# Optimization experiments

Hardware: AMD Instinct MI355X
Metric: run time of the kernel (lower is better)

Reference implementation:

```python
import jax, jax.numpy as jnp
import numpy as np

N_POS = 8192          # number of positive samples
N_NEG = 4000          # negatives per positive
N_TOT = N_POS + N_POS * N_NEG


def setup_inputs() -> dict:
    key = jax.random.key(0)
    k1, k2 = jax.random.split(key)
    predict_val = jax.random.normal(k1, (N_TOT,), dtype=jnp.float32)
    # 'index' is a permutation; the module reorders predict_val by argsort(index)
    index = jax.random.permutation(k2, jnp.arange(N_TOT, dtype=jnp.int64))
    return {"predict_val": predict_val, "index": index, "num": N_NEG, "num_pos": N_POS}


def reference(predict_val, index, num, num_pos):
    # index_tuple = sorted(enumerate(index)) by value -> reorder by argsort(index)
    pv = predict_val[jnp.argsort(index)]
    pos = pv[:num_pos]                                  # [num_pos]
    neg = pv[num_pos:num_pos + num_pos * num]
    neg = neg.reshape(num_pos, num)                     # [num_pos, num]
    # rank of pos among {neg, pos} sorted descending == 1 + #(neg > pos)
    # (ties are randomly broken in the original; measure-zero for continuous scores)
    rank = 1 + jnp.sum(neg > pos[:, None], axis=-1)     # [num_pos], int
    sample_mrr = 1.0 / rank.astype(pv.dtype)            # [num_pos]
    mrr = jnp.mean(sample_mrr)
    return mrr, sample_mrr
```

## Files before the change

### kernel.cpp

```cpp
#include <hip/hip_runtime.h>


constexpr int N_POS = 8192;
constexpr int N_NEG = 4000;
constexpr int NSLOT = N_POS / 4;
constexpr int GRID  = 256;
constexpr int BLK   = 1024;
constexpr int NTHR  = GRID * BLK;
constexpr int NITER = 32;
constexpr int CNT_BLOCKS = 512;

typedef int   vint4   __attribute__((ext_vector_type(4)));
typedef float vfloat4 __attribute__((ext_vector_type(4)));
typedef unsigned int u32;
typedef unsigned long long u64;

__global__ __launch_bounds__(BLK, 4) void fused_mrr_kernel(
    const vint4* __restrict__ idx4, const float* __restrict__ pvs,
    float* __restrict__ pos, u64* __restrict__ cnt, u32* __restrict__ bar,
    float* __restrict__ out, int nvec) {
  __shared__ float pos_lds[N_POS];
  __shared__ u32   lcnt[N_POS];
  __shared__ float wsum[BLK / 64];
  __shared__ int   is_last;
  const int tid = threadIdx.x;
  const int gid = blockIdx.x * BLK + tid;
  const vfloat4* __restrict__ pv4 = (const vfloat4*)pvs;

#pragma unroll
  for (int i = 0; i < N_POS / BLK; ++i) lcnt[tid + i * BLK] = 0u;
  if (gid <= NSLOT) (void)atomicExch(&cnt[gid], 0ull);

  u32 code[2 * NITER];
#define PA_ELEM(VX, PIDX, CO)                                            \
  {                                                                      \
    u32 c_ = ((VX) >= N_POS) ? ((u32)((VX)-N_POS) / (u32)N_NEG)          \
                             : 0xFFFFu;                                  \
    if ((VX) < N_POS) (void)atomicExch(&pos[VX], pvs[PIDX]);             \
    (CO) = c_;                                                           \
  }
#pragma unroll
  for (int i = 0; i < NITER; ++i) {
    const int j = gid + i * NTHR;
    if (j < nvec) {
      vint4 v = __builtin_nontemporal_load(&idx4[j]);
      u32 c0, c1, c2, c3;
      PA_ELEM(v.x, 4 * j + 0, c0)
      PA_ELEM(v.y, 4 * j + 1, c1)
      PA_ELEM(v.z, 4 * j + 2, c2)
      PA_ELEM(v.w, 4 * j + 3, c3)
      code[2 * i]     = c0 | (c1 << 16);
      code[2 * i + 1] = c2 | (c3 << 16);
    } else {
      code[2 * i]     = 0xFFFFFFFFu;
      code[2 * i + 1] = 0xFFFFFFFFu;
    }
  }
  for (int j = gid + NITER * NTHR; j < nvec; j += NTHR) {
    vint4 v = idx4[j];
    u32 dummy;
    PA_ELEM(v.x, 4 * j + 0, dummy)
    PA_ELEM(v.y, 4 * j + 1, dummy)
    PA_ELEM(v.z, 4 * j + 2, dummy)
    PA_ELEM(v.w, 4 * j + 3, dummy)
    (void)dummy;
  }
#undef PA_ELEM

  __builtin_amdgcn_s_waitcnt(0);
  __syncthreads();
  if (tid == 0) {
    __hip_atomic_fetch_add(bar, 1u, __ATOMIC_RELAXED,
                           __HIP_MEMORY_SCOPE_AGENT);
    while (__hip_atomic_load(bar, __ATOMIC_RELAXED,
                             __HIP_MEMORY_SCOPE_AGENT) < (u32)GRID)
      __builtin_amdgcn_s_sleep(4);
  }
  __syncthreads();

#pragma unroll
  for (int i = 0; i < N_POS / BLK; ++i) {
    const int s = tid + i * BLK;
    pos_lds[s] = __hip_atomic_load(&pos[s], __ATOMIC_RELAXED,
                                   __HIP_MEMORY_SCOPE_AGENT);
  }
  __syncthreads();

#define PB_ELEM(R, XV)                                                   \
  if ((R) < (u32)N_POS && (XV) > pos_lds[R]) atomicAdd(&lcnt[R], 1u);
#pragma unroll
  for (int i = 0; i < NITER; ++i) {
    const int j = gid + i * NTHR;
    if (j < nvec) {
      vfloat4 x = __builtin_nontemporal_load(&pv4[j]);
      u32 w0 = code[2 * i], w1 = code[2 * i + 1];
      u32 r0 = w0 & 0xFFFFu, r1 = w0 >> 16;
      u32 r2 = w1 & 0xFFFFu, r3 = w1 >> 16;
      PB_ELEM(r0, x.x)
      PB_ELEM(r1, x.y)
      PB_ELEM(r2, x.z)
      PB_ELEM(r3, x.w)
    }
  }
  for (int j = gid + NITER * NTHR; j < nvec; j += NTHR) {
    vint4 v = idx4[j];
    vfloat4 x = pv4[j];
    u32 r0 = (v.x >= N_POS) ? ((u32)(v.x - N_POS) / (u32)N_NEG) : 0xFFFFu;
    u32 r1 = (v.y >= N_POS) ? ((u32)(v.y - N_POS) / (u32)N_NEG) : 0xFFFFu;
    u32 r2 = (v.z >= N_POS) ? ((u32)(v.z - N_POS) / (u32)N_NEG) : 0xFFFFu;
    u32 r3 = (v.w >= N_POS) ? ((u32)(v.w - N_POS) / (u32)N_NEG) : 0xFFFFu;
    PB_ELEM(r0, x.x)
    PB_ELEM(r1, x.y)
    PB_ELEM(r2, x.z)
    PB_ELEM(r3, x.w)
  }
#undef PB_ELEM
  __syncthreads();

  for (int s = tid; s < NSLOT; s += BLK) {
    u32 c0 = lcnt[4 * s + 0], c1 = lcnt[4 * s + 1];
    u32 c2 = lcnt[4 * s + 2], c3 = lcnt[4 * s + 3];
    u64 p = (u64)c0 | ((u64)c1 << 16) | ((u64)c2 << 32) | ((u64)c3 << 48);
    if (p) atomicAdd(&cnt[s], p);
  }

  __builtin_amdgcn_s_waitcnt(0);
  __syncthreads();
  if (tid == 0) {
    u64 prev = __hip_atomic_fetch_add(&cnt[NSLOT], 1ull, __ATOMIC_RELAXED,
                                      __HIP_MEMORY_SCOPE_AGENT);
    is_last = (prev == (u64)(GRID - 1));
  }
  __syncthreads();
  if (!is_last) return;

  float lsum = 0.f;
  for (int s = tid; s < NSLOT; s += BLK) {
    u64 p = __hip_atomic_load(&cnt[s], __ATOMIC_RELAXED,
                              __HIP_MEMORY_SCOPE_AGENT);
    float m0 = 1.0f / (float)(1u + (u32)(p & 0xFFFFu));
    float m1 = 1.0f / (float)(1u + (u32)((p >> 16) & 0xFFFFu));
    float m2 = 1.0f / (float)(1u + (u32)((p >> 32) & 0xFFFFu));
    float m3 = 1.0f / (float)(1u + (u32)((p >> 48) & 0xFFFFu));
    vfloat4 m = {m0, m1, m2, m3};
    *(vfloat4*)&out[1 + 4 * s] = m;
    lsum += m0 + m1 + m2 + m3;
  }
#pragma unroll
  for (int off = 32; off > 0; off >>= 1) lsum += __shfl_down(lsum, off, 64);
  if ((tid & 63) == 0) wsum[tid >> 6] = lsum;
  __syncthreads();
  if (tid == 0) {
    float tot = 0.f;
#pragma unroll
    for (int w = 0; w < BLK / 64; ++w) tot += wsum[w];
    out[0] = tot / (float)N_POS;
  }
}

__global__ __launch_bounds__(256) void scatter_pos_kernel(
    const vint4* __restrict__ idx4, const float* __restrict__ pv,
    float* __restrict__ pos, u64* __restrict__ cnt, int nvec) {
  const int gtid = blockIdx.x * 256 + threadIdx.x;
  if (gtid <= NSLOT) cnt[gtid] = 0ull;
  const int stride = gridDim.x * 256;
  int j = gtid;
#define SC_ELEM(V, JJ)                                   \
  if ((V).x < N_POS) pos[(V).x] = pv[4 * (JJ) + 0];      \
  if ((V).y < N_POS) pos[(V).y] = pv[4 * (JJ) + 1];      \
  if ((V).z < N_POS) pos[(V).z] = pv[4 * (JJ) + 2];      \
  if ((V).w < N_POS) pos[(V).w] = pv[4 * (JJ) + 3];
  for (; j + stride < nvec; j += 2 * stride) {
    vint4 a = idx4[j];
    vint4 b = idx4[j + stride];
    SC_ELEM(a, j)
    SC_ELEM(b, j + stride)
  }
  for (; j < nvec; j += stride) {
    vint4 a = idx4[j];
    SC_ELEM(a, j)
  }
#undef SC_ELEM
}

__global__ __launch_bounds__(1024) void count_kernel(
    const vint4* __restrict__ idx4, const vfloat4* __restrict__ pv4,
    const float* __restrict__ pos, u64* __restrict__ cnt,
    float* __restrict__ out, int nvec) {
  __shared__ float pos_lds[N_POS];
  __shared__ u32   lcnt[N_POS];
  __shared__ float wsum[16];
  __shared__ int is_last;
  for (int i = threadIdx.x; i < N_POS; i += 1024) {
    pos_lds[i] = pos[i];
    lcnt[i] = 0u;
  }
  __syncthreads();

  const int stride = gridDim.x * 1024;
  int j = blockIdx.x * 1024 + threadIdx.x;
#define CT_ELEM(IV, XV)                                              \
  if ((IV) >= N_POS) {                                               \
    unsigned r = (unsigned)((IV) - N_POS) / (unsigned)N_NEG;         \
    if ((XV) > pos_lds[r]) atomicAdd(&lcnt[r], 1u);                  \
  }
#define CT_VEC(V, X)                                                 \
  CT_ELEM((V).x, (X).x) CT_ELEM((V).y, (X).y)                        \
  CT_ELEM((V).z, (X).z) CT_ELEM((V).w, (X).w)
  for (; j + stride < nvec; j += 2 * stride) {
    vint4 va = idx4[j];
    vint4 vb = idx4[j + stride];
    vfloat4 xa = __builtin_nontemporal_load(&pv4[j]);
    vfloat4 xb = __builtin_nontemporal_load(&pv4[j + stride]);
    CT_VEC(va, xa)
    CT_VEC(vb, xb)
  }
  for (; j < nvec; j += stride) {
    vint4 va = idx4[j];
    vfloat4 xa = __builtin_nontemporal_load(&pv4[j]);
    CT_VEC(va, xa)
  }
#undef CT_VEC
#undef CT_ELEM
  __syncthreads();

  for (int s = threadIdx.x; s < NSLOT; s += 1024) {
    u32 c0 = lcnt[4 * s + 0], c1 = lcnt[4 * s + 1];
    u32 c2 = lcnt[4 * s + 2], c3 = lcnt[4 * s + 3];
    u64 p = (u64)c0 | ((u64)c1 << 16) | ((u64)c2 << 32) | ((u64)c3 << 48);
    if (p) atomicAdd(&cnt[s], p);
  }

  __builtin_amdgcn_s_waitcnt(0);
  __syncthreads();
  if (threadIdx.x == 0) {
    u64 prev = __hip_atomic_fetch_add(&cnt[NSLOT], 1ull, __ATOMIC_RELAXED,
                                      __HIP_MEMORY_SCOPE_AGENT);
    is_last = (prev == (u64)(gridDim.x - 1));
  }
  __syncthreads();
  if (!is_last) return;

  float lsum = 0.f;
  for (int s = threadIdx.x; s < NSLOT; s += 1024) {
    u64 p = __hip_atomic_load(&cnt[s], __ATOMIC_RELAXED,
                              __HIP_MEMORY_SCOPE_AGENT);
    float m0 = 1.0f / (float)(1u + (u32)(p & 0xFFFFu));
    float m1 = 1.0f / (float)(1u + (u32)((p >> 16) & 0xFFFFu));
    float m2 = 1.0f / (float)(1u + (u32)((p >> 32) & 0xFFFFu));
    float m3 = 1.0f / (float)(1u + (u32)((p >> 48) & 0xFFFFu));
    vfloat4 m = {m0, m1, m2, m3};
    *(vfloat4*)&out[1 + 4 * s] = m;
    lsum += m0 + m1 + m2 + m3;
  }
#pragma unroll
  for (int off = 32; off > 0; off >>= 1) lsum += __shfl_down(lsum, off, 64);
  if ((threadIdx.x & 63) == 0) wsum[threadIdx.x >> 6] = lsum;
  __syncthreads();
  if (threadIdx.x == 0) {
    float tot = 0.f;
#pragma unroll
    for (int w = 0; w < 16; ++w) tot += wsum[w];
    out[0] = tot / (float)N_POS;
  }
}

extern "C" void kernel_launch(void* const* d_in, const int* in_sizes, int n_in,
                              void* d_out, int out_size, void* d_ws,
                              size_t ws_size, hipStream_t stream) {
  const float* pv = (const float*)d_in[0];
  const vint4* idx4 = (const vint4*)d_in[1];
  float* out = (float*)d_out;
  float* pos = (float*)d_ws;
  u64* cnt = (u64*)((char*)d_ws + 32 * 1024);
  u32* bar = (u32*)((char*)d_ws + 56 * 1024);
  int nvec = in_sizes[0] / 4;

  hipMemsetAsync(bar, 0, sizeof(u32), stream);

  void* args[] = {(void*)&idx4, (void*)&pv, (void*)&pos, (void*)&cnt,
                  (void*)&bar,  (void*)&out, (void*)&nvec};
  hipError_t e = hipLaunchCooperativeKernel((const void*)fused_mrr_kernel,
                                            dim3(GRID), dim3(BLK), args, 0,
                                            stream);
  if (e != hipSuccess) {
    scatter_pos_kernel<<<2048, 256, 0, stream>>>(idx4, pv, pos, cnt, nvec);
    count_kernel<<<CNT_BLOCKS, 1024, 0, stream>>>(idx4, (const vfloat4*)pv,
                                                  pos, cnt, out, nvec);
  }
}
```

Measured before the change: 312.9 us.

## Reload index array in count phase instead of caching packed row codes in registers

Measured after the change: 316.7 us. No clear change (+1.2%).

```diff
diff --git a/kernel.cpp b/kernel.cpp
--- a/kernel.cpp
+++ b/kernel.cpp
@@ -6,8 +6,6 @@
 constexpr int NSLOT = N_POS / 4;
 constexpr int GRID  = 256;
 constexpr int BLK   = 1024;
-constexpr int NTHR  = GRID * BLK;
-constexpr int NITER = 32;
 constexpr int CNT_BLOCKS = 512;
 
 typedef int   vint4   __attribute__((ext_vector_type(4)));
@@ -25,47 +23,32 @@
   __shared__ int   is_last;
   const int tid = threadIdx.x;
   const int gid = blockIdx.x * BLK + tid;
+  const int stride = GRID * BLK;
   const vfloat4* __restrict__ pv4 = (const vfloat4*)pvs;
 
 #pragma unroll
   for (int i = 0; i < N_POS / BLK; ++i) lcnt[tid + i * BLK] = 0u;
   if (gid <= NSLOT) (void)atomicExch(&cnt[gid], 0ull);
 
-  u32 code[2 * NITER];
-#define PA_ELEM(VX, PIDX, CO)                                            \
-  {                                                                      \
-    u32 c_ = ((VX) >= N_POS) ? ((u32)((VX)-N_POS) / (u32)N_NEG)          \
-                             : 0xFFFFu;                                  \
-    if ((VX) < N_POS) (void)atomicExch(&pos[VX], pvs[PIDX]);             \
-    (CO) = c_;                                                           \
-  }
-#pragma unroll
-  for (int i = 0; i < NITER; ++i) {
-    const int j = gid + i * NTHR;
-    if (j < nvec) {
-      vint4 v = __builtin_nontemporal_load(&idx4[j]);
-      u32 c0, c1, c2, c3;
-      PA_ELEM(v.x, 4 * j + 0, c0)
-      PA_ELEM(v.y, 4 * j + 1, c1)
-      PA_ELEM(v.z, 4 * j + 2, c2)
-      PA_ELEM(v.w, 4 * j + 3, c3)
-      code[2 * i]     = c0 | (c1 << 16);
-      code[2 * i + 1] = c2 | (c3 << 16);
-    } else {
-      code[2 * i]     = 0xFFFFFFFFu;
-      code[2 * i + 1] = 0xFFFFFFFFu;
-    }
-  }
-  for (int j = gid + NITER * NTHR; j < nvec; j += NTHR) {
-    vint4 v = idx4[j];
-    u32 dummy;
-    PA_ELEM(v.x, 4 * j + 0, dummy)
-    PA_ELEM(v.y, 4 * j + 1, dummy)
-    PA_ELEM(v.z, 4 * j + 2, dummy)
-    PA_ELEM(v.w, 4 * j + 3, dummy)
-    (void)dummy;
-  }
-#undef PA_ELEM
+  {
+    int j = gid;
+#define SC_ELEM(V, JJ)                                               \
+  if ((V).x < N_POS) (void)atomicExch(&pos[(V).x], pvs[4 * (JJ) + 0]); \
+  if ((V).y < N_POS) (void)atomicExch(&pos[(V).y], pvs[4 * (JJ) + 1]); \
+  if ((V).z < N_POS) (void)atomicExch(&pos[(V).z], pvs[4 * (JJ) + 2]); \
+  if ((V).w < N_POS) (void)atomicExch(&pos[(V).w], pvs[4 * (JJ) + 3]);
+    for (; j + stride < nvec; j += 2 * stride) {
+      vint4 a = idx4[j];
+      vint4 b = idx4[j + stride];
+      SC_ELEM(a, j)
+      SC_ELEM(b, j + stride)
+    }
+    for (; j < nvec; j += stride) {
+      vint4 a = idx4[j];
+      SC_ELEM(a, j)
+    }
+#undef SC_ELEM
+  }
 
   __builtin_amdgcn_s_waitcnt(0);
   __syncthreads();
@@ -86,35 +69,32 @@
   }
   __syncthreads();
 
-#define PB_ELEM(R, XV)                                                   \
-  if ((R) < (u32)N_POS && (XV) > pos_lds[R]) atomicAdd(&lcnt[R], 1u);
-#pragma unroll
-  for (int i = 0; i < NITER; ++i) {
-    const int j = gid + i * NTHR;
-    if (j < nvec) {
-      vfloat4 x = __builtin_nontemporal_load(&pv4[j]);
-      u32 w0 = code[2 * i], w1 = code[2 * i + 1];
-      u32 r0 = w0 & 0xFFFFu, r1 = w0 >> 16;
-      u32 r2 = w1 & 0xFFFFu, r3 = w1 >> 16;
-      PB_ELEM(r0, x.x)
-      PB_ELEM(r1, x.y)
-      PB_ELEM(r2, x.z)
-      PB_ELEM(r3, x.w)
-    }
-  }
-  for (int j = gid + NITER * NTHR; j < nvec; j += NTHR) {
-    vint4 v = idx4[j];
-    vfloat4 x = pv4[j];
-    u32 r0 = (v.x >= N_POS) ? ((u32)(v.x - N_POS) / (u32)N_NEG) : 0xFFFFu;
-    u32 r1 = (v.y >= N_POS) ? ((u32)(v.y - N_POS) / (u32)N_NEG) : 0xFFFFu;
-    u32 r2 = (v.z >= N_POS) ? ((u32)(v.z - N_POS) / (u32)N_NEG) : 0xFFFFu;
-    u32 r3 = (v.w >= N_POS) ? ((u32)(v.w - N_POS) / (u32)N_NEG) : 0xFFFFu;
-    PB_ELEM(r0, x.x)
-    PB_ELEM(r1, x.y)
-    PB_ELEM(r2, x.z)
-    PB_ELEM(r3, x.w)
-  }
-#undef PB_ELEM
+  {
+    int j = gid;
+#define CT_ELEM(IV, XV)                                              \
+  if ((IV) >= N_POS) {                                               \
+    unsigned r = (unsigned)((IV) - N_POS) / (unsigned)N_NEG;         \
+    if ((XV) > pos_lds[r]) atomicAdd(&lcnt[r], 1u);                  \
+  }
+#define CT_VEC(V, X)                                                 \
+  CT_ELEM((V).x, (X).x) CT_ELEM((V).y, (X).y)                        \
+  CT_ELEM((V).z, (X).z) CT_ELEM((V).w, (X).w)
+    for (; j + stride < nvec; j += 2 * stride) {
+      vint4 va = idx4[j];
+      vint4 vb = idx4[j + stride];
+      vfloat4 xa = __builtin_nontemporal_load(&pv4[j]);
+      vfloat4 xb = __builtin_nontemporal_load(&pv4[j + stride]);
+      CT_VEC(va, xa)
+      CT_VEC(vb, xb)
+    }
+    for (; j < nvec; j += stride) {
+      vint4 va = idx4[j];
+      vfloat4 xa = __builtin_nontemporal_load(&pv4[j]);
+      CT_VEC(va, xa)
+    }
+#undef CT_VEC
+#undef CT_ELEM
+  }
   __syncthreads();
 
   for (int s = tid; s < NSLOT; s += BLK) {
```
